# Kernel optimization log

Hardware: AMD Instinct MI355X
Metric: run time of the kernel (lower is better)

The kernel has to match this reference:

```python
import jax, jax.numpy as jnp
import numpy as np

EMB, HEADS, DEPTH, SEQ, BATCH = 256, 8, 4, 8192, 4
DH = EMB // HEADS  # 32
FF = 4 * EMB
EPS = 1e-5


def setup_inputs() -> dict:
    key = jax.random.key(0)
    ks = jax.random.split(key, 8)
    w = lambda k, shape: jax.random.normal(k, shape, dtype=jnp.float32) * 0.02
    D = DEPTH
    return {
        "x": jax.random.normal(ks[0], (BATCH, SEQ, EMB), dtype=jnp.float32),
        "Wq": w(ks[1], (D, EMB, EMB)),
        "Wk": w(ks[2], (D, EMB, EMB)),
        "Wv": w(ks[3], (D, EMB, EMB)),
        "Wo": w(ks[4], (D, EMB, EMB)),
        "bo": jnp.zeros((D, EMB), jnp.float32),
        "ln1_g": jnp.ones((D, EMB), jnp.float32),
        "ln1_b": jnp.zeros((D, EMB), jnp.float32),
        "W1": w(ks[5], (D, EMB, FF)),
        "b1": jnp.zeros((D, FF), jnp.float32),
        "W2": w(ks[6], (D, FF, EMB)),
        "b2": jnp.zeros((D, EMB), jnp.float32),
        "ln2_g": jnp.ones((D, EMB), jnp.float32),
        "ln2_b": jnp.zeros((D, EMB), jnp.float32),
    }


def _layernorm(x, g, b):
    mu = x.mean(-1, keepdims=True)
    var = ((x - mu) ** 2).mean(-1, keepdims=True)
    return (x - mu) * jax.lax.rsqrt(var + EPS) * g + b


def _linear_attn(x, Wq, Wk, Wv, Wo, bo):
    # lucidrains linear_attn: q,k scaled by d**-0.25; softmax q over feature dim,
    # k over sequence dim; context = k^T v (per head), out = q @ context.
    b, n, dm = x.shape
    split = lambda t: t.reshape(b, n, HEADS, DH).transpose(0, 2, 1, 3)  # -> bhnd
    scale = DH ** -0.25
    q = jax.nn.softmax(split(x @ Wq) * scale, axis=-1)   # over d
    k = jax.nn.softmax(split(x @ Wk) * scale, axis=-2)   # over n
    v = split(x @ Wv)
    context = jnp.einsum('bhnd,bhne->bhde', k, v)        # [b,h,d,d]
    out = jnp.einsum('bhnd,bhde->bhne', q, context)      # [b,h,n,d]
    out = out.transpose(0, 2, 1, 3).reshape(b, n, dm)
    return out @ Wo + bo


def _forward(x, Wq, Wk, Wv, Wo, bo, ln1_g, ln1_b, W1, b1, W2, b2, ln2_g, ln2_b):
    for i in range(DEPTH):
        h = _layernorm(x, ln1_g[i], ln1_b[i])
        x = x + _linear_attn(h, Wq[i], Wk[i], Wv[i], Wo[i], bo[i])
        h = _layernorm(x, ln2_g[i], ln2_b[i])
        x = x + (jax.nn.gelu(h @ W1[i] + b1[i], approximate=False) @ W2[i] + b2[i])
    return x


def reference(x, Wq, Wk, Wv, Wo, bo, ln1_g, ln1_b, W1, b1, W2, b2, ln2_g, ln2_b):
    return _forward(x, Wq, Wk, Wv, Wo, bo, ln1_g, ln1_b, W1, b1, W2, b2, ln2_g, ln2_b)
```

## Files before the change

### kernel.cpp

```cpp
#include <hip/hip_runtime.h>
#include <hip/hip_bf16.h>

typedef __attribute__((ext_vector_type(8))) short bf16x8;
typedef __attribute__((ext_vector_type(4))) float f32x4;

#define EMB 256
#define HEADS 8
#define DH 32
#define SEQ 8192
#define BATCH 4
#define NROWS (SEQ*BATCH)
#define FFD 1024
#define DEPTH 4
#define QKVN 768
#define SCALE 0.42044820762685725f
#define NCHUNK 128
#define ROWS_PER_CHUNK (SEQ/NCHUNK)

static __device__ __forceinline__ float bf2f(ushort u){
  union { unsigned int i; float f; } x; x.i = ((unsigned int)u) << 16; return x.f;
}
static __device__ __forceinline__ ushort f2bf(float f){
  union { __hip_bfloat16 h; ushort u; } cv;
  cv.h = __float2bfloat16(f);
  return cv.u;
}
static __device__ __forceinline__ float gelu_f(float v){
  float y = 0.7978845608028654f * (v + 0.044715f*v*v*v);
  float e = __expf(2.0f*y);
  return 0.5f*v*(1.0f + (1.0f - 2.0f/(e + 1.0f)));
}

static __device__ __forceinline__ void gload_lds16(const ushort* g, ushort* l){
  __builtin_amdgcn_global_load_lds(
      (const __attribute__((address_space(1))) unsigned int*)(uintptr_t)g,
      (__attribute__((address_space(3))) unsigned int*)(uintptr_t)l,
      16, 0, 0);
}

__global__ __launch_bounds__(256) void prep_weights(
    const float* __restrict__ Wq, const float* __restrict__ Wk,
    const float* __restrict__ Wv, const float* __restrict__ Wo,
    const float* __restrict__ W1, const float* __restrict__ W2,
    ushort* __restrict__ wqkv_t, ushort* __restrict__ wo_t,
    ushort* __restrict__ w1_t, ushort* __restrict__ w2_t)
{
  __shared__ float tile[32][33];
  int bid = blockIdx.x;
  int L = bid / 768, r = bid % 768;
  const float* src; ushort* dst; int K, N, tidx;
  if (r < 192){ int which = r >> 6; tidx = r & 63;
    src = (which==0?Wq:which==1?Wk:Wv) + (long)L*65536;
    dst = wqkv_t + (long)L*QKVN*EMB + which*EMB*EMB; K=256; N=256;
  } else if (r < 256){ tidx = r-192; src = Wo + (long)L*65536; dst = wo_t + (long)L*65536; K=256; N=256; }
  else if (r < 512){ tidx = r-256; src = W1 + (long)L*262144; dst = w1_t + (long)L*262144; K=256; N=1024; }
  else { tidx = r-512; src = W2 + (long)L*262144; dst = w2_t + (long)L*262144; K=1024; N=256; }
  int tn = N >> 5;
  int tk = tidx / tn, tj = tidx % tn;
  int k0 = tk*32, n0 = tj*32;
  int c = threadIdx.x & 31, r0 = threadIdx.x >> 5;
  #pragma unroll
  for (int i=0;i<4;i++){
    int rr = r0 + i*8;
    tile[rr][c] = src[(long)(k0+rr)*N + n0 + c];
  }
  __syncthreads();
  #pragma unroll
  for (int i=0;i<4;i++){
    int rr = r0 + i*8;
    dst[(long)(n0+rr)*K + k0 + c] = f2bf(tile[c][rr]);
  }
}

__global__ __launch_bounds__(256) void ln_kernel(const float* __restrict__ x,
    const float* __restrict__ g, const float* __restrict__ bb,
    ushort* __restrict__ h)
{
  int wid = threadIdx.x >> 6, lane = threadIdx.x & 63;
  long row = (long)blockIdx.x*4 + wid;
  const float4 xv = *(const float4*)(x + row*EMB + lane*4);
  float s = xv.x+xv.y+xv.z+xv.w;
  float s2 = xv.x*xv.x+xv.y*xv.y+xv.z*xv.z+xv.w*xv.w;
  #pragma unroll
  for (int m=1;m<64;m<<=1){ s += __shfl_xor(s,m,64); s2 += __shfl_xor(s2,m,64); }
  float mean = s * (1.0f/EMB);
  float inv = rsqrtf(s2*(1.0f/EMB) - mean*mean + 1e-5f);
  float4 gv = *(const float4*)(g + lane*4);
  float4 bv = *(const float4*)(bb + lane*4);
  ushort4 o;
  o.x = f2bf((xv.x-mean)*inv*gv.x + bv.x);
  o.y = f2bf((xv.y-mean)*inv*gv.y + bv.y);
  o.z = f2bf((xv.z-mean)*inv*gv.z + bv.z);
  o.w = f2bf((xv.w-mean)*inv*gv.w + bv.w);
  *(ushort4*)(h + row*EMB + lane*4) = o;
}

template<int MODE, int BM, int BN, int BK>
__global__ __launch_bounds__(512, 2) void gemm_bt(
    const ushort* __restrict__ A, const ushort* __restrict__ Bt,
    int M, int N, int K,
    const float* __restrict__ bias,
    const float* __restrict__ xinf, const ushort* __restrict__ xinb,
    float* __restrict__ xoutf, ushort* __restrict__ xoutb,
    ushort* __restrict__ outb,
    const float* __restrict__ lng, const float* __restrict__ lnb)
{
  constexpr int NF = BN/64;
  constexpr int MR = BM/32;
  constexpr int MH = MR/4;
  constexpr int KK = BK/32;
  constexpr int CPR = BK/8;
  constexpr int AI = BM*BK/4096;
  constexpr int BI = BN*BK/4096;
  constexpr int TI = AI + BI;
  constexpr int NPH = KK*MH;
  __shared__ ushort LDSraw[2*BM*BK + 2*BN*BK];
  ushort* Abuf0 = LDSraw;
  ushort* Abuf1 = LDSraw + BM*BK;
  ushort* Bbuf0 = LDSraw + 2*BM*BK;
  ushort* Bbuf1 = LDSraw + 2*BM*BK + BN*BK;
  int t = threadIdx.x;
  int lane = t & 63, wid = t >> 6;
  int wr = wid >> 2, wc = wid & 3;
  int wrb = wr*(BM/2), wcb = wc*(BN/4);
  long rowA0 = (long)blockIdx.x * BM;
  long colB0 = (long)blockIdx.y * BN;
  const ushort* gA[AI]; int dA[AI];
  #pragma unroll
  for (int i=0;i<AI;i++){
    int l = i*512 + t;
    int row = l / CPR;
    int clog = (t % CPR) ^ (row & (CPR-1));
    gA[i] = A + (rowA0 + row)*(long)K + clog*8;
    dA[i] = l*8;
  }
  const ushort* gB[BI]; int dB[BI];
  #pragma unroll
  for (int i=0;i<BI;i++){
    int l = i*512 + t;
    int row = l / CPR;
    int clog = (t % CPR) ^ (row & (CPR-1));
    gB[i] = Bt + (colB0 + row)*(long)K + clog*8;
    dB[i] = l*8;
  }
  ushort* Ac = Abuf0; ushort* An = Abuf1;
  ushort* Bc = Bbuf0; ushort* Bn = Bbuf1;
  f32x4 acc[MR][NF] = {};
  int fr = lane & 15, cr4 = lane >> 4;
  int nsteps = K / BK;
  #pragma unroll
  for (int i=0;i<AI;i++) gload_lds16(gA[i], Ac + dA[i]);
  #pragma unroll
  for (int i=0;i<BI;i++) gload_lds16(gB[i], Bc + dB[i]);
  asm volatile("s_waitcnt vmcnt(0)" ::: "memory");
  __syncthreads();
  for (int s = 0; s < nsteps; ++s){
    bool pf = (s+1 < nsteps);
    long knext = (long)(s+1) * BK;
    #pragma unroll
    for (int kk=0; kk<KK; ++kk){
      int chunk = (((kk*4 + cr4)) ^ (fr & (CPR-1))) << 3;
      bf16x8 bv[NF];
      #pragma unroll
      for (int n=0;n<NF;n++)
        bv[n] = *(const bf16x8*)(Bc + (wcb + n*16 + fr)*BK + chunk);
      #pragma unroll
      for (int mh=0; mh<MH; ++mh){
        int sp = kk*MH + mh;
        bf16x8 av[4];
        #pragma unroll
        for (int m=0;m<4;m++)
          av[m] = *(const bf16x8*)(Ac + (wrb + (mh*4+m)*16 + fr)*BK + chunk);
        if (pf){
          #pragma unroll
          for (int j=0;j<TI;j++){
            if (j*NPH >= sp*TI && j*NPH < (sp+1)*TI){
              if (j < AI) gload_lds16(gA[j]+knext, An+dA[j]);
              else        gload_lds16(gB[j-AI]+knext, Bn+dB[j-AI]);
            }
          }
        }
        __builtin_amdgcn_s_setprio(1);
        #pragma unroll
        for (int m=0;m<4;m++){
          #pragma unroll
          for (int n=0;n<NF;n++)
            acc[mh*4+m][n] = __builtin_amdgcn_mfma_f32_16x16x32_bf16(av[m], bv[n], acc[mh*4+m][n], 0,0,0);
        }
        __builtin_amdgcn_s_setprio(0);
      }
    }
    asm volatile("s_waitcnt vmcnt(0)" ::: "memory");
    __syncthreads();
    ushort* tp;
    tp = Ac; Ac = An; An = tp;
    tp = Bc; Bc = Bn; Bn = tp;
  }
  constexpr int BNP = BN + 4;
  constexpr int ROUNDS = BM/32;
  constexpr int RPH = BM/64;
  float* bounce = (float*)LDSraw;
  int fq = lane >> 4;
  constexpr int TPR = BN/4;
  int rdrow = t / TPR;
  int rdcol = (t % TPR) * 4;
  constexpr int RPP = 512 / TPR;
  constexpr int PASSES = 32 / RPP;
  #pragma unroll
  for (int r = 0; r < ROUNDS; ++r){
    __syncthreads();
    if (wr == r / RPH){
      int mb = (r % RPH)*2;
      #pragma unroll
      for (int m4=0;m4<2;m4++){
        #pragma unroll
        for (int n=0;n<NF;n++){
          #pragma unroll
          for (int i=0;i<4;i++)
            bounce[(m4*16 + fq*4 + i)*BNP + wcb + n*16 + fr] = acc[mb+m4][n][i];
        }
      }
    }
    __syncthreads();
    long gr0 = rowA0 + r*32;
    #pragma unroll
    for (int p=0;p<PASSES;p++){
      int lr = p*RPP + rdrow;
      long gr = gr0 + lr;
      long gc = colB0 + rdcol;
      float4 v = *(float4*)&bounce[lr*BNP + rdcol];
      if (MODE==0){
        ushort4 o; o.x=f2bf(v.x); o.y=f2bf(v.y); o.z=f2bf(v.z); o.w=f2bf(v.w);
        *(ushort4*)&outb[gr*N + gc] = o;
      } else if (MODE==2){
        const float4 bv4 = *(const float4*)&bias[gc];
        ushort4 o;
        o.x = f2bf(gelu_f(v.x + bv4.x)); o.y = f2bf(gelu_f(v.y + bv4.y));
        o.z = f2bf(gelu_f(v.z + bv4.z)); o.w = f2bf(gelu_f(v.w + bv4.w));
        *(ushort4*)&outb[gr*N + gc] = o;
      } else {
        const float4 bv4 = *(const float4*)&bias[gc];
        float xo0, xo1, xo2, xo3;
        if (MODE==3){
          const float4 xo = *(const float4*)&xinf[gr*N + gc];
          xo0=xo.x; xo1=xo.y; xo2=xo.z; xo3=xo.w;
        } else {
          const ushort4 xb = *(const ushort4*)&xinb[gr*N + gc];
          xo0=bf2f(xb.x); xo1=bf2f(xb.y); xo2=bf2f(xb.z); xo3=bf2f(xb.w);
        }
        v.x += bv4.x + xo0; v.y += bv4.y + xo1;
        v.z += bv4.z + xo2; v.w += bv4.w + xo3;
        ushort4 xw;
        xw.x=f2bf(v.x); xw.y=f2bf(v.y); xw.z=f2bf(v.z); xw.w=f2bf(v.w);
        *(ushort4*)&xoutb[gr*N + gc] = xw;
        float s1 = v.x+v.y+v.z+v.w;
        float s2 = v.x*v.x+v.y*v.y+v.z*v.z+v.w*v.w;
        #pragma unroll
        for (int mm=1;mm<64;mm<<=1){ s1 += __shfl_xor(s1,mm,64); s2 += __shfl_xor(s2,mm,64); }
        float mean = s1 * (1.0f/EMB);
        float inv = rsqrtf(s2*(1.0f/EMB) - mean*mean + 1e-5f);
        const float4 g4 = *(const float4*)&lng[gc];
        const float4 b4 = *(const float4*)&lnb[gc];
        ushort4 o;
        o.x = f2bf((v.x-mean)*inv*g4.x + b4.x);
        o.y = f2bf((v.y-mean)*inv*g4.y + b4.y);
        o.z = f2bf((v.z-mean)*inv*g4.z + b4.z);
        o.w = f2bf((v.w-mean)*inv*g4.w + b4.w);
        *(ushort4*)&outb[gr*EMB + gc] = o;
      }
    }
  }
}

template<int MODE>
__global__ __launch_bounds__(512) void ff_fused(
    const ushort* __restrict__ A, const ushort* __restrict__ w1t,
    const ushort* __restrict__ w2t,
    const float* __restrict__ b1, const float* __restrict__ b2,
    const ushort* __restrict__ xinb,
    float* __restrict__ xoutf, ushort* __restrict__ xoutb,
    ushort* __restrict__ hout,
    const float* __restrict__ lng, const float* __restrict__ lnb)
{
  __shared__ ushort As[128*256];
  __shared__ ushort W1b[64*256];
  __shared__ ushort W2b[256*64];
  __shared__ ushort Ps[128*68];
  int t = threadIdx.x, lane = t & 63, wid = t >> 6;
  int fr = lane & 15, cr4 = lane >> 4, fq = lane >> 4;
  long rowA0 = (long)blockIdx.x * 128;
  #pragma unroll
  for (int i=0;i<8;i++){
    int l = i*512 + t;
    int row = l >> 5;
    int clog = (l & 31) ^ (row & 31);
    gload_lds16(A + (rowA0+row)*256 + clog*8, As + l*8);
  }
  #pragma unroll
  for (int i=0;i<4;i++){
    int l = i*512 + t;
    int row = l >> 5;
    int clog = (l & 31) ^ (row & 31);
    gload_lds16(w1t + row*256 + clog*8, W1b + l*8);
  }
  asm volatile("s_waitcnt vmcnt(0)" ::: "memory");
  __syncthreads();
  int rwP = (wid & 3)*32, fwP = (wid >> 2)*32;
  int rw2 = (wid >> 2)*64, cw2 = (wid & 3)*64;
  f32x4 accC[4][4] = {};
  for (int j = 0; j < 16; ++j){
    f32x4 accP[2][2] = {};
    #pragma unroll
    for (int kk=0; kk<8; ++kk){
      if ((kk & 1) == 0){
        int i = kk >> 1;
        int l = i*512 + t;
        int row = l >> 3, c = l & 7;
        int clog = c ^ (row & 7);
        gload_lds16(w2t + row*1024 + j*64 + clog*8, W2b + l*8);
      }
      int ci = kk*4 + cr4;
      bf16x8 av[2], wv[2];
      #pragma unroll
      for (int m=0;m<2;m++){
        int row = rwP + m*16 + fr;
        av[m] = *(const bf16x8*)(As + row*256 + ((ci ^ (row&31)) << 3));
      }
      #pragma unroll
      for (int n=0;n<2;n++){
        int row = fwP + n*16 + fr;
        wv[n] = *(const bf16x8*)(W1b + row*256 + ((ci ^ (row&31)) << 3));
      }
      __builtin_amdgcn_s_setprio(1);
      #pragma unroll
      for (int m=0;m<2;m++){
        #pragma unroll
        for (int n=0;n<2;n++)
          accP[m][n] = __builtin_amdgcn_mfma_f32_16x16x32_bf16(av[m], wv[n], accP[m][n], 0,0,0);
      }
      __builtin_amdgcn_s_setprio(0);
    }
    #pragma unroll
    for (int n=0;n<2;n++){
      float bv = b1[j*64 + fwP + n*16 + fr];
      #pragma unroll
      for (int m=0;m<2;m++){
        #pragma unroll
        for (int i2=0;i2<4;i2++){
          int row = rwP + m*16 + fq*4 + i2;
          Ps[row*68 + fwP + n*16 + fr] = f2bf(gelu_f(accP[m][n][i2] + bv));
        }
      }
    }
    asm volatile("s_waitcnt vmcnt(0)" ::: "memory");
    __syncthreads();
    bool pw1 = (j+1 < 16);
    #pragma unroll
    for (int kk2=0; kk2<2; ++kk2){
      if (pw1){
        #pragma unroll
        for (int i=0;i<2;i++){
          int ii = kk2*2 + i;
          int l = ii*512 + t;
          int row = l >> 5;
          int clog = (l & 31) ^ (row & 31);
          gload_lds16(w1t + (long)(j+1)*64*256 + row*256 + clog*8, W1b + l*8);
        }
      }
      int ci2 = kk2*4 + cr4;
      bf16x8 pv[4], wv2[4];
      #pragma unroll
      for (int m=0;m<4;m++){
        int row = rw2 + m*16 + fr;
        pv[m] = *(const bf16x8*)(Ps + row*68 + ci2*8);
      }
      #pragma unroll
      for (int n=0;n<4;n++){
        int row = cw2 + n*16 + fr;
        wv2[n] = *(const bf16x8*)(W2b + row*64 + ((ci2 ^ (row&7)) << 3));
      }
      __builtin_amdgcn_s_setprio(1);
      #pragma unroll
      for (int m=0;m<4;m++){
        #pragma unroll
        for (int n=0;n<4;n++)
          accC[m][n] = __builtin_amdgcn_mfma_f32_16x16x32_bf16(pv[m], wv2[n], accC[m][n], 0,0,0);
      }
      __builtin_amdgcn_s_setprio(0);
    }
    asm volatile("s_waitcnt vmcnt(0)" ::: "memory");
    __syncthreads();
  }
  float* bounce = (float*)As;
  int rdrow = t >> 6;
  int rdcol = (t & 63) * 4;
  #pragma unroll
  for (int r = 0; r < 4; ++r){
    __syncthreads();
    if ((wid >> 2) == (r >> 1)){
      int mb = (r & 1)*2;
      #pragma unroll
      for (int m4=0;m4<2;m4++){
        #pragma unroll
        for (int n=0;n<4;n++){
          #pragma unroll
          for (int i2=0;i2<4;i2++)
            bounce[(m4*16 + fq*4 + i2)*260 + cw2 + n*16 + fr] = accC[mb+m4][n][i2];
        }
      }
    }
    __syncthreads();
    long gr0 = rowA0 + r*32;
    #pragma unroll
    for (int p=0;p<4;p++){
      int lr = p*8 + rdrow;
      long gr = gr0 + lr;
      long gc = rdcol;
      float4 v = *(float4*)&bounce[lr*260 + rdcol];
      const float4 bv4 = *(const float4*)&b2[gc];
      const ushort4 xb4 = *(const ushort4*)&xinb[gr*EMB + gc];
      v.x += bv4.x + bf2f(xb4.x); v.y += bv4.y + bf2f(xb4.y);
      v.z += bv4.z + bf2f(xb4.z); v.w += bv4.w + bf2f(xb4.w);
      if (MODE==5){
        *(float4*)&xoutf[gr*EMB + gc] = v;
      } else {
        ushort4 xw;
        xw.x=f2bf(v.x); xw.y=f2bf(v.y); xw.z=f2bf(v.z); xw.w=f2bf(v.w);
        *(ushort4*)&xoutb[gr*EMB + gc] = xw;
        float s1 = v.x+v.y+v.z+v.w;
        float s2 = v.x*v.x+v.y*v.y+v.z*v.z+v.w*v.w;
        #pragma unroll
        for (int mm=1;mm<64;mm<<=1){ s1 += __shfl_xor(s1,mm,64); s2 += __shfl_xor(s2,mm,64); }
        float mean = s1 * (1.0f/EMB);
        float inv = rsqrtf(s2*(1.0f/EMB) - mean*mean + 1e-5f);
        const float4 g4 = *(const float4*)&lng[gc];
        const float4 b4 = *(const float4*)&lnb[gc];
        ushort4 o;
        o.x = f2bf((v.x-mean)*inv*g4.x + b4.x);
        o.y = f2bf((v.y-mean)*inv*g4.y + b4.y);
        o.z = f2bf((v.z-mean)*inv*g4.z + b4.z);
        o.w = f2bf((v.w-mean)*inv*g4.w + b4.w);
        *(ushort4*)&hout[gr*EMB + gc] = o;
      }
    }
  }
}

__global__ __launch_bounds__(256) void colstats_partial(const ushort* __restrict__ qkv,
    float* __restrict__ pmax, float* __restrict__ psum)
{
  int ch = blockIdx.x, b = blockIdx.y;
  int t = threadIdx.x;
  const ushort* base = qkv + ((long)b*SEQ + (long)ch*ROWS_PER_CHUNK)*QKVN + EMB + t;
  float m[4] = {-1e30f,-1e30f,-1e30f,-1e30f};
  float s[4] = {0.f,0.f,0.f,0.f};
  #pragma unroll 2
  for (int n = 0; n < ROWS_PER_CHUNK; n += 4){
    #pragma unroll
    for (int j=0;j<4;j++){
      float v = bf2f(base[(long)(n+j)*QKVN]) * SCALE;
      float m2 = fmaxf(m[j], v);
      s[j] = s[j]*__expf(m[j]-m2) + __expf(v-m2);
      m[j] = m2;
    }
  }
  float M = fmaxf(fmaxf(m[0],m[1]), fmaxf(m[2],m[3]));
  float S = s[0]*__expf(m[0]-M) + s[1]*__expf(m[1]-M)
          + s[2]*__expf(m[2]-M) + s[3]*__expf(m[3]-M);
  long idx = ((long)b*NCHUNK + ch)*EMB + t;
  pmax[idx] = M; psum[idx] = S;
}

__global__ __launch_bounds__(256) void colstats_reduce(const float* __restrict__ pmax,
    const float* __restrict__ psum, float* __restrict__ kmax, float* __restrict__ ksum)
{
  int b = blockIdx.x, t = threadIdx.x;
  const float* pm = pmax + (long)b*NCHUNK*EMB + t;
  const float* ps = psum + (long)b*NCHUNK*EMB + t;
  float m = -1e30f, s = 0.f;
  for (int c = 0; c < NCHUNK; ++c){
    float cm = pm[(long)c*EMB], cs = ps[(long)c*EMB];
    float m2 = fmaxf(m, cm);
    s = s*__expf(m-m2) + cs*__expf(cm-m2);
    m = m2;
  }
  kmax[b*EMB + t] = m;
  ksum[b*EMB + t] = s;
}

__global__ __launch_bounds__(256) void ctx_partial(
    const ushort* __restrict__ qkv, const float* __restrict__ kmax,
    float* __restrict__ ctx_part)
{
  constexpr int LT = 72;
  __shared__ ushort ekT[32*LT];
  __shared__ ushort vvT[32*LT];
  int ch = blockIdx.x, h = blockIdx.y, b = blockIdx.z;
  int t = threadIdx.x, lane = t & 63, wid = t >> 6;
  long nbase = (long)b*SEQ + ch*512;
  int lrow = t >> 2, lseg = (t & 3) << 3;
  float km[8];
  #pragma unroll
  for (int j=0;j<8;j++) km[j] = kmax[b*256 + h*DH + lseg + j];
  int wstep = wid & 1, wdr = (wid >> 1) << 4;
  f32x4 acc0 = {}, acc1 = {};
  int frow = lane & 15, g8 = (lane >> 4) << 3;
  for (int st = 0; st < 8; ++st){
    long n0 = nbase + st*64;
    const ushort* gk = qkv + (n0 + lrow)*QKVN + EMB + h*DH + lseg;
    uint4 kv = *(const uint4*)gk;
    uint4 vv = *(const uint4*)(gk + EMB);
    __syncthreads();
    const ushort* kp = (const ushort*)&kv;
    const ushort* vp = (const ushort*)&vv;
    #pragma unroll
    for (int j=0;j<8;j++){
      float f = bf2f(kp[j])*SCALE;
      ekT[(lseg+j)*LT + lrow] = f2bf(__expf(f - km[j]));
      vvT[(lseg+j)*LT + lrow] = vp[j];
    }
    __syncthreads();
    bf16x8 afr = *(const bf16x8*)(ekT + (wdr + frow)*LT + wstep*32 + g8);
    bf16x8 bf0 = *(const bf16x8*)(vvT + frow*LT + wstep*32 + g8);
    bf16x8 bf1 = *(const bf16x8*)(vvT + (16 + frow)*LT + wstep*32 + g8);
    acc0 = __builtin_amdgcn_mfma_f32_16x16x32_bf16(afr, bf0, acc0, 0,0,0);
    acc1 = __builtin_amdgcn_mfma_f32_16x16x32_bf16(afr, bf1, acc1, 0,0,0);
  }
  int fq = lane >> 4;
  long pb = (((long)(b*HEADS+h))*32 + (ch*2+wstep))*1024;
  #pragma unroll
  for (int i=0;i<4;i++){
    ctx_part[pb + (wdr + fq*4 + i)*32 + frow] = acc0[i];
    ctx_part[pb + (wdr + fq*4 + i)*32 + 16 + frow] = acc1[i];
  }
}

__global__ __launch_bounds__(256) void ctx_reduce(const float* __restrict__ ctx_part,
    const float* __restrict__ ksum, ushort* __restrict__ ctxT)
{
  int bh = blockIdx.x; int b = bh >> 3, h = bh & 7;
  int t = threadIdx.x; int d = t >> 3, e4 = (t & 7) << 2;
  const float* p = ctx_part + (long)bh*32768 + d*32 + e4;
  float sx=0, sy=0, sz=0, sw=0;
  for (int c=0;c<32;c++){
    const float4 v = *(const float4*)(p + c*1024);
    sx+=v.x; sy+=v.y; sz+=v.z; sw+=v.w;
  }
  float inv = 1.0f / ksum[b*256 + h*DH + d];
  long base = (long)bh*1024;
  ctxT[base + (e4+0)*32 + d] = f2bf(sx*inv);
  ctxT[base + (e4+1)*32 + d] = f2bf(sy*inv);
  ctxT[base + (e4+2)*32 + d] = f2bf(sz*inv);
  ctxT[base + (e4+3)*32 + d] = f2bf(sw*inv);
}

__global__ __launch_bounds__(256) void attn_out(
    const ushort* __restrict__ qkv, const ushort* __restrict__ ctxT,
    ushort* __restrict__ ao)
{
  __shared__ ushort sq[4][16][264];
  int t = threadIdx.x, lane = t & 63, wid = t >> 6;
  long row0 = (long)blockIdx.x*64 + wid*16;
  int b = (int)(row0 / SEQ);
  int fr = lane & 15, g = lane >> 4;
  bf16x8 cf[8][2];
  #pragma unroll
  for (int h=0;h<8;h++){
    #pragma unroll
    for (int eh=0;eh<2;eh++)
      cf[h][eh] = *(const bf16x8*)(ctxT + ((long)(b*8+h)*32 + eh*16 + fr)*32 + g*8);
  }
  long gr = row0 + fr;
  #pragma unroll
  for (int hh=0;hh<2;hh++){
    int h = g*2 + hh;
    const ushort* qp = qkv + gr*QKVN + h*DH;
    union { uint4 v[4]; ushort u[32]; } qq;
    qq.v[0]=*(const uint4*)qp; qq.v[1]=*(const uint4*)(qp+8);
    qq.v[2]=*(const uint4*)(qp+16); qq.v[3]=*(const uint4*)(qp+24);
    float f[32]; float m = -1e30f;
    #pragma unroll
    for (int j=0;j<32;j++){ f[j] = bf2f(qq.u[j])*SCALE; m = fmaxf(m, f[j]); }
    float ssum = 0.f;
    #pragma unroll
    for (int j=0;j<32;j++){ f[j] = __expf(f[j]-m); ssum += f[j]; }
    float inv = 1.0f/ssum;
    union { uint4 v[4]; ushort u[32]; } oo;
    #pragma unroll
    for (int j=0;j<32;j++) oo.u[j] = f2bf(f[j]*inv);
    ushort* dst = &sq[wid][fr][h*DH];
    #pragma unroll
    for (int c2=0;c2<4;c2++) *(uint4*)(dst + c2*8) = oo.v[c2];
  }
  __syncthreads();
  #pragma unroll
  for (int h=0;h<8;h++){
    bf16x8 af = *(const bf16x8*)(&sq[wid][fr][h*DH + g*8]);
    f32x4 z = {};
    f32x4 o0 = __builtin_amdgcn_mfma_f32_16x16x32_bf16(af, cf[h][0], z, 0,0,0);
    f32x4 o1 = __builtin_amdgcn_mfma_f32_16x16x32_bf16(af, cf[h][1], z, 0,0,0);
    #pragma unroll
    for (int i=0;i<4;i++){
      long r = row0 + g*4 + i;
      ao[r*EMB + h*DH + fr]      = f2bf(o0[i]);
      ao[r*EMB + h*DH + 16 + fr] = f2bf(o1[i]);
    }
  }
}

extern "C" void kernel_launch(void* const* d_in, const int* in_sizes, int n_in,
                              void* d_out, int out_size, void* d_ws, size_t ws_size,
                              hipStream_t stream)
{
  const float* x_in = (const float*)d_in[0];
  const float* Wq  = (const float*)d_in[1];
  const float* Wk  = (const float*)d_in[2];
  const float* Wv  = (const float*)d_in[3];
  const float* Wo  = (const float*)d_in[4];
  const float* bo  = (const float*)d_in[5];
  const float* ln1g = (const float*)d_in[6];
  const float* ln1b = (const float*)d_in[7];
  const float* W1  = (const float*)d_in[8];
  const float* b1  = (const float*)d_in[9];
  const float* W2  = (const float*)d_in[10];
  const float* b2  = (const float*)d_in[11];
  const float* ln2g = (const float*)d_in[12];
  const float* ln2b = (const float*)d_in[13];
  float* xout = (float*)d_out;

  char* ws = (char*)d_ws;
  ushort* h_buf  = (ushort*)ws;  ws += (long)NROWS*EMB*2;
  ushort* xb     = (ushort*)ws;  ws += (long)NROWS*EMB*2;
  ushort* big    = (ushort*)ws;  ws += (long)NROWS*FFD*2;
  ushort* wqkv_t = (ushort*)ws;  ws += (long)DEPTH*QKVN*EMB*2;
  ushort* wo_t   = (ushort*)ws;  ws += (long)DEPTH*EMB*EMB*2;
  ushort* w1_t   = (ushort*)ws;  ws += (long)DEPTH*FFD*EMB*2;
  ushort* w2_t   = (ushort*)ws;  ws += (long)DEPTH*EMB*FFD*2;
  float*  kmax   = (float*)ws;   ws += (long)BATCH*EMB*4;
  float*  ksumv  = (float*)ws;   ws += (long)BATCH*EMB*4;
  float*  ctx_part = (float*)ws; ws += (long)BATCH*HEADS*32*1024*4;
  ushort* ctxT   = (ushort*)ws;  ws += (long)BATCH*HEADS*1024*2;
  float*  pmax   = (float*)ws;   ws += (long)BATCH*NCHUNK*EMB*4;
  float*  psum   = (float*)ws;   ws += (long)BATCH*NCHUNK*EMB*4;

  prep_weights<<<3072, 256, 0, stream>>>(Wq, Wk, Wv, Wo, W1, W2, wqkv_t, wo_t, w1_t, w2_t);
  ln_kernel<<<NROWS/4, 256, 0, stream>>>(x_in, ln1g, ln1b, h_buf);

  ushort* qkv = big;
  for (int L = 0; L < DEPTH; ++L){
    gemm_bt<0,128,128,64><<<dim3(NROWS/128, QKVN/128), 512, 0, stream>>>(
        h_buf, wqkv_t + (long)L*QKVN*EMB, NROWS, QKVN, EMB,
        nullptr, nullptr, nullptr, nullptr, nullptr, qkv, nullptr, nullptr);
    colstats_partial<<<dim3(NCHUNK, BATCH), 256, 0, stream>>>(qkv, pmax, psum);
    colstats_reduce<<<BATCH, 256, 0, stream>>>(pmax, psum, kmax, ksumv);
    ctx_partial<<<dim3(16, HEADS, BATCH), 256, 0, stream>>>(qkv, kmax, ctx_part);
    ctx_reduce<<<32, 256, 0, stream>>>(ctx_part, ksumv, ctxT);
    attn_out<<<NROWS/64, 256, 0, stream>>>(qkv, ctxT, h_buf);
    if (L == 0){
      gemm_bt<3,128,256,64><<<dim3(NROWS/128, 1), 512, 0, stream>>>(
          h_buf, wo_t, NROWS, EMB, EMB,
          bo, x_in, nullptr, nullptr, xb, h_buf, ln2g, ln2b);
    } else {
      gemm_bt<4,128,256,64><<<dim3(NROWS/128, 1), 512, 0, stream>>>(
          h_buf, wo_t + (long)L*EMB*EMB, NROWS, EMB, EMB,
          bo + L*EMB, nullptr, xb, nullptr, xb, h_buf,
          ln2g + L*EMB, ln2b + L*EMB);
    }
    if (L + 1 < DEPTH){
      ff_fused<4><<<256, 512, 0, stream>>>(
          h_buf, w1_t + (long)L*FFD*EMB, w2_t + (long)L*EMB*FFD,
          b1 + L*FFD, b2 + L*EMB, xb, nullptr, xb, h_buf,
          ln1g + (L+1)*EMB, ln1b + (L+1)*EMB);
    } else {
      ff_fused<5><<<256, 512, 0, stream>>>(
          h_buf, w1_t + (long)L*FFD*EMB, w2_t + (long)L*EMB*FFD,
          b1 + L*FFD, b2 + L*EMB, xb, xout, nullptr, nullptr,
          nullptr, nullptr);
    }
  }
}
```

Measured before the change: 582.8 us.

## Swap QKV GEMM grid order, hoist epilogue params, front-load W2/W1 prefetches

The QKV GEMM grid now puts column tiles on blockIdx.x, so the six column tiles of one row block launch next to each other and share the A rows in cache. Bias, LayerNorm gamma/beta and b1/b2 loads are hoisted out of the epilogue and inner loops in both gemm_bt and ff_fused. The W2 chunk loads in ff_fused are moved into the first four k-steps, and the next W1 prefetch is issued all at once in the first kk2 iteration. The goal is better L2 reuse and fewer redundant loads, at the cost of longer-lived registers and more bursty memory issue.

```diff
diff --git a/kernel.cpp b/kernel.cpp
--- a/kernel.cpp
+++ b/kernel.cpp
@@ -95,7 +95,7 @@
   *(ushort4*)(h + row*EMB + lane*4) = o;
 }
 
-template<int MODE, int BM, int BN, int BK>
+template<int MODE, int BM, int BN, int BK, int GSWAP>
 __global__ __launch_bounds__(512, 2) void gemm_bt(
     const ushort* __restrict__ A, const ushort* __restrict__ Bt,
     int M, int N, int K,
@@ -123,8 +123,9 @@
   int lane = t & 63, wid = t >> 6;
   int wr = wid >> 2, wc = wid & 3;
   int wrb = wr*(BM/2), wcb = wc*(BN/4);
-  long rowA0 = (long)blockIdx.x * BM;
-  long colB0 = (long)blockIdx.y * BN;
+  long rowA0, colB0;
+  if (GSWAP){ rowA0 = (long)blockIdx.y * BM; colB0 = (long)blockIdx.x * BN; }
+  else      { rowA0 = (long)blockIdx.x * BM; colB0 = (long)blockIdx.y * BN; }
   const ushort* gA[AI]; int dA[AI];
   #pragma unroll
   for (int i=0;i<AI;i++){
@@ -206,6 +207,10 @@
   int rdcol = (t % TPR) * 4;
   constexpr int RPP = 512 / TPR;
   constexpr int PASSES = 32 / RPP;
+  long gcf = colB0 + rdcol;
+  float4 bv4e = {0,0,0,0}, g4e = {0,0,0,0}, b4e = {0,0,0,0};
+  if (MODE==2 || MODE==3 || MODE==4) bv4e = *(const float4*)&bias[gcf];
+  if (MODE==3 || MODE==4){ g4e = *(const float4*)&lng[gcf]; b4e = *(const float4*)&lnb[gcf]; }
   #pragma unroll
   for (int r = 0; r < ROUNDS; ++r){
     __syncthreads();
@@ -227,46 +232,41 @@
     for (int p=0;p<PASSES;p++){
       int lr = p*RPP + rdrow;
       long gr = gr0 + lr;
-      long gc = colB0 + rdcol;
       float4 v = *(float4*)&bounce[lr*BNP + rdcol];
       if (MODE==0){
         ushort4 o; o.x=f2bf(v.x); o.y=f2bf(v.y); o.z=f2bf(v.z); o.w=f2bf(v.w);
-        *(ushort4*)&outb[gr*N + gc] = o;
+        *(ushort4*)&outb[gr*N + gcf] = o;
       } else if (MODE==2){
-        const float4 bv4 = *(const float4*)&bias[gc];
         ushort4 o;
-        o.x = f2bf(gelu_f(v.x + bv4.x)); o.y = f2bf(gelu_f(v.y + bv4.y));
-        o.z = f2bf(gelu_f(v.z + bv4.z)); o.w = f2bf(gelu_f(v.w + bv4.w));
-        *(ushort4*)&outb[gr*N + gc] = o;
+        o.x = f2bf(gelu_f(v.x + bv4e.x)); o.y = f2bf(gelu_f(v.y + bv4e.y));
+        o.z = f2bf(gelu_f(v.z + bv4e.z)); o.w = f2bf(gelu_f(v.w + bv4e.w));
+        *(ushort4*)&outb[gr*N + gcf] = o;
       } else {
-        const float4 bv4 = *(const float4*)&bias[gc];
         float xo0, xo1, xo2, xo3;
         if (MODE==3){
-          const float4 xo = *(const float4*)&xinf[gr*N + gc];
+          const float4 xo = *(const float4*)&xinf[gr*N + gcf];
           xo0=xo.x; xo1=xo.y; xo2=xo.z; xo3=xo.w;
         } else {
-          const ushort4 xb = *(const ushort4*)&xinb[gr*N + gc];
+          const ushort4 xb = *(const ushort4*)&xinb[gr*N + gcf];
           xo0=bf2f(xb.x); xo1=bf2f(xb.y); xo2=bf2f(xb.z); xo3=bf2f(xb.w);
         }
-        v.x += bv4.x + xo0; v.y += bv4.y + xo1;
-        v.z += bv4.z + xo2; v.w += bv4.w + xo3;
+        v.x += bv4e.x + xo0; v.y += bv4e.y + xo1;
+        v.z += bv4e.z + xo2; v.w += bv4e.w + xo3;
         ushort4 xw;
         xw.x=f2bf(v.x); xw.y=f2bf(v.y); xw.z=f2bf(v.z); xw.w=f2bf(v.w);
-        *(ushort4*)&xoutb[gr*N + gc] = xw;
+        *(ushort4*)&xoutb[gr*N + gcf] = xw;
         float s1 = v.x+v.y+v.z+v.w;
         float s2 = v.x*v.x+v.y*v.y+v.z*v.z+v.w*v.w;
         #pragma unroll
         for (int mm=1;mm<64;mm<<=1){ s1 += __shfl_xor(s1,mm,64); s2 += __shfl_xor(s2,mm,64); }
         float mean = s1 * (1.0f/EMB);
         float inv = rsqrtf(s2*(1.0f/EMB) - mean*mean + 1e-5f);
-        const float4 g4 = *(const float4*)&lng[gc];
-        const float4 b4 = *(const float4*)&lnb[gc];
         ushort4 o;
-        o.x = f2bf((v.x-mean)*inv*g4.x + b4.x);
-        o.y = f2bf((v.y-mean)*inv*g4.y + b4.y);
-        o.z = f2bf((v.z-mean)*inv*g4.z + b4.z);
-        o.w = f2bf((v.w-mean)*inv*g4.w + b4.w);
-        *(ushort4*)&outb[gr*EMB + gc] = o;
+        o.x = f2bf((v.x-mean)*inv*g4e.x + b4e.x);
+        o.y = f2bf((v.y-mean)*inv*g4e.y + b4e.y);
+        o.z = f2bf((v.z-mean)*inv*g4e.z + b4e.z);
+        o.w = f2bf((v.w-mean)*inv*g4e.w + b4e.w);
+        *(ushort4*)&outb[gr*EMB + gcf] = o;
       }
     }
   }
@@ -309,12 +309,13 @@
   int rw2 = (wid >> 2)*64, cw2 = (wid & 3)*64;
   f32x4 accC[4][4] = {};
   for (int j = 0; j < 16; ++j){
+    float bvp0 = b1[j*64 + fwP + fr];
+    float bvp1 = b1[j*64 + fwP + 16 + fr];
     f32x4 accP[2][2] = {};
     #pragma unroll
     for (int kk=0; kk<8; ++kk){
-      if ((kk & 1) == 0){
-        int i = kk >> 1;
-        int l = i*512 + t;
+      if (kk < 4){
+        int l = kk*512 + t;
         int row = l >> 3, c = l & 7;
         int clog = c ^ (row & 7);
         gload_lds16(w2t + row*1024 + j*64 + clog*8, W2b + l*8);
@@ -342,7 +343,7 @@
     }
     #pragma unroll
     for (int n=0;n<2;n++){
-      float bv = b1[j*64 + fwP + n*16 + fr];
+      float bv = (n==0) ? bvp0 : bvp1;
       #pragma unroll
       for (int m=0;m<2;m++){
         #pragma unroll
@@ -357,10 +358,9 @@
     bool pw1 = (j+1 < 16);
     #pragma unroll
     for (int kk2=0; kk2<2; ++kk2){
-      if (pw1){
-        #pragma unroll
-        for (int i=0;i<2;i++){
-          int ii = kk2*2 + i;
+      if (pw1 && kk2==0){
+        #pragma unroll
+        for (int ii=0;ii<4;ii++){
           int l = ii*512 + t;
           int row = l >> 5;
           int clog = (l & 31) ^ (row & 31);
@@ -394,6 +394,9 @@
   float* bounce = (float*)As;
   int rdrow = t >> 6;
   int rdcol = (t & 63) * 4;
+  const float4 bv4 = *(const float4*)&b2[rdcol];
+  float4 g4 = {0,0,0,0}, b4 = {0,0,0,0};
+  if (MODE==4){ g4 = *(const float4*)&lng[rdcol]; b4 = *(const float4*)&lnb[rdcol]; }
   #pragma unroll
   for (int r = 0; r < 4; ++r){
     __syncthreads();
@@ -415,32 +418,28 @@
     for (int p=0;p<4;p++){
       int lr = p*8 + rdrow;
       long gr = gr0 + lr;
-      long gc = rdcol;
       float4 v = *(float4*)&bounce[lr*260 + rdcol];
-      const float4 bv4 = *(const float4*)&b2[gc];
-      const ushort4 xb4 = *(const ushort4*)&xinb[gr*EMB + gc];
+      const ushort4 xb4 = *(const ushort4*)&xinb[gr*EMB + rdcol];
       v.x += bv4.x + bf2f(xb4.x); v.y += bv4.y + bf2f(xb4.y);
       v.z += bv4.z + bf2f(xb4.z); v.w += bv4.w + bf2f(xb4.w);
       if (MODE==5){
-        *(float4*)&xoutf[gr*EMB + gc] = v;
+        *(float4*)&xoutf[gr*EMB + rdcol] = v;
       } else {
         ushort4 xw;
         xw.x=f2bf(v.x); xw.y=f2bf(v.y); xw.z=f2bf(v.z); xw.w=f2bf(v.w);
-        *(ushort4*)&xoutb[gr*EMB + gc] = xw;
+        *(ushort4*)&xoutb[gr*EMB + rdcol] = xw;
         float s1 = v.x+v.y+v.z+v.w;
         float s2 = v.x*v.x+v.y*v.y+v.z*v.z+v.w*v.w;
         #pragma unroll
         for (int mm=1;mm<64;mm<<=1){ s1 += __shfl_xor(s1,mm,64); s2 += __shfl_xor(s2,mm,64); }
         float mean = s1 * (1.0f/EMB);
         float inv = rsqrtf(s2*(1.0f/EMB) - mean*mean + 1e-5f);
-        const float4 g4 = *(const float4*)&lng[gc];
-        const float4 b4 = *(const float4*)&lnb[gc];
         ushort4 o;
         o.x = f2bf((v.x-mean)*inv*g4.x + b4.x);
         o.y = f2bf((v.y-mean)*inv*g4.y + b4.y);
         o.z = f2bf((v.z-mean)*inv*g4.z + b4.z);
         o.w = f2bf((v.w-mean)*inv*g4.w + b4.w);
-        *(ushort4*)&hout[gr*EMB + gc] = o;
+        *(ushort4*)&hout[gr*EMB + rdcol] = o;
       }
     }
   }
@@ -648,7 +647,7 @@
 
   ushort* qkv = big;
   for (int L = 0; L < DEPTH; ++L){
-    gemm_bt<0,128,128,64><<<dim3(NROWS/128, QKVN/128), 512, 0, stream>>>(
+    gemm_bt<0,128,128,64,1><<<dim3(QKVN/128, NROWS/128), 512, 0, stream>>>(
         h_buf, wqkv_t + (long)L*QKVN*EMB, NROWS, QKVN, EMB,
         nullptr, nullptr, nullptr, nullptr, nullptr, qkv, nullptr, nullptr);
     colstats_partial<<<dim3(NCHUNK, BATCH), 256, 0, stream>>>(qkv, pmax, psum);
@@ -657,11 +656,11 @@
     ctx_reduce<<<32, 256, 0, stream>>>(ctx_part, ksumv, ctxT);
     attn_out<<<NROWS/64, 256, 0, stream>>>(qkv, ctxT, h_buf);
     if (L == 0){
-      gemm_bt<3,128,256,64><<<dim3(NROWS/128, 1), 512, 0, stream>>>(
+      gemm_bt<3,128,256,64,0><<<dim3(NROWS/128, 1), 512, 0, stream>>>(
           h_buf, wo_t, NROWS, EMB, EMB,
           bo, x_in, nullptr, nullptr, xb, h_buf, ln2g, ln2b);
     } else {
-      gemm_bt<4,128,256,64><<<dim3(NROWS/128, 1), 512, 0, stream>>>(
+      gemm_bt<4,128,256,64,0><<<dim3(NROWS/128, 1), 512, 0, stream>>>(
           h_buf, wo_t + (long)L*EMB*EMB, NROWS, EMB, EMB,
           bo + L*EMB, nullptr, xb, nullptr, xb, h_buf,
           ln2g + L*EMB, ln2b + L*EMB);
```

Result: no change. 582.5 us (median of 2 runs) (-0.0%).
